# Optimization experiments

Hardware: AMD Instinct MI355X
Metric: run time of the kernel (lower is better)

## Reference

```python
import jax, jax.numpy as jnp
import numpy as np

N = 500_000
CHANNELS = 256
NUM_GRAPHS = 2048


def setup_inputs() -> dict:
    key = jax.random.key(0)
    k1, k2, k3 = jax.random.split(key, 3)
    features = jax.random.normal(k1, (N, CHANNELS), dtype=jnp.float32)
    batch = jnp.sort(jax.random.randint(k2, (N,), 0, NUM_GRAPHS, dtype=jnp.int64))
    batch = batch.at[-1].set(NUM_GRAPHS - 1)  # pin max so num_segments == NUM_GRAPHS
    W_att = jax.random.normal(k3, (CHANNELS, 1), dtype=jnp.float32) * (1.0 / np.sqrt(CHANNELS))
    b_att = jnp.zeros((1,), dtype=jnp.float32)
    return {"features": features, "batch": batch, "W_att": W_att, "b_att": b_att}


def reference(features, batch, W_att, b_att):
    # attention: Linear(channels, 1) -> Sigmoid, per node  [N, 1]
    weights = jax.nn.sigmoid(features @ W_att + b_att)
    # weighted per-graph sum: equivalent to the python loop over batch ids,
    # fused as a single segment reduction. num_segments = batch.max()+1 = NUM_GRAPHS.
    weighted = features * weights  # [N, C]
    out = jax.ops.segment_sum(weighted, batch, num_segments=NUM_GRAPHS)  # [B, C]
    return out
```

## Files before the change

kernel.cpp:

```cpp
#include <hip/hip_runtime.h>


constexpr int kChannels  = 256;
constexpr int kVecPerRow = kChannels / 4;

typedef float vfloat4 __attribute__((ext_vector_type(4)));

__device__ inline int lower_bound_i32(const int* __restrict__ b, int n, int v) {
    int lo = 0, hi = n;
    while (lo < hi) {
        int mid = (lo + hi) >> 1;
        if (b[mid] < v) lo = mid + 1; else hi = mid;
    }
    return lo;
}

__device__ inline float sigmoidf(float x) {
    return 1.0f / (1.0f + __expf(-x));
}

__global__ void hgp_seg_kernel(const float* __restrict__ features,
                               const int*   __restrict__ batch,
                               const float* __restrict__ W_att,
                               const float* __restrict__ b_att,
                               float*       __restrict__ out,
                               int n_nodes) {
    const int g    = blockIdx.x;
    const int wv   = threadIdx.x >> 6;
    const int lane = threadIdx.x & 63;

    const int seg_start = lower_bound_i32(batch, n_nodes, g);
    const int seg_end   = lower_bound_i32(batch, n_nodes, g + 1);
    const int seg_len   = seg_end - seg_start;

    const int q   = (seg_len + 3) >> 2;
    const int ws_ = seg_start + wv * q;
    const int we_ = min(ws_ + q, seg_end);

    const float4 w4  = reinterpret_cast<const float4*>(W_att)[lane];
    const float bias = b_att[0];
    const vfloat4* __restrict__ frow = reinterpret_cast<const vfloat4*>(features);

    float ax = 0.f, ay = 0.f, az = 0.f, aw = 0.f;

    int n = ws_;
    for (; n + 4 <= we_; n += 4) {
        const size_t base = (size_t)n * kVecPerRow + lane;
        vfloat4 r0 = __builtin_nontemporal_load(&frow[base]);
        vfloat4 r1 = __builtin_nontemporal_load(&frow[base + 1 * kVecPerRow]);
        vfloat4 r2 = __builtin_nontemporal_load(&frow[base + 2 * kVecPerRow]);
        vfloat4 r3 = __builtin_nontemporal_load(&frow[base + 3 * kVecPerRow]);

        float p0 = r0[0] * w4.x + r0[1] * w4.y + r0[2] * w4.z + r0[3] * w4.w;
        float p1 = r1[0] * w4.x + r1[1] * w4.y + r1[2] * w4.z + r1[3] * w4.w;
        float p2 = r2[0] * w4.x + r2[1] * w4.y + r2[2] * w4.z + r2[3] * w4.w;
        float p3 = r3[0] * w4.x + r3[1] * w4.y + r3[2] * w4.z + r3[3] * w4.w;

        #pragma unroll
        for (int off = 32; off > 0; off >>= 1) {
            p0 += __shfl_xor(p0, off, 64);
            p1 += __shfl_xor(p1, off, 64);
            p2 += __shfl_xor(p2, off, 64);
            p3 += __shfl_xor(p3, off, 64);
        }

        const float g0 = sigmoidf(p0 + bias);
        const float g1 = sigmoidf(p1 + bias);
        const float g2 = sigmoidf(p2 + bias);
        const float g3 = sigmoidf(p3 + bias);

        ax += r0[0] * g0 + r1[0] * g1 + r2[0] * g2 + r3[0] * g3;
        ay += r0[1] * g0 + r1[1] * g1 + r2[1] * g2 + r3[1] * g3;
        az += r0[2] * g0 + r1[2] * g1 + r2[2] * g2 + r3[2] * g3;
        aw += r0[3] * g0 + r1[3] * g1 + r2[3] * g2 + r3[3] * g3;
    }
    for (; n < we_; ++n) {
        vfloat4 r = __builtin_nontemporal_load(&frow[(size_t)n * kVecPerRow + lane]);
        float p = r[0] * w4.x + r[1] * w4.y + r[2] * w4.z + r[3] * w4.w;
        #pragma unroll
        for (int off = 32; off > 0; off >>= 1) p += __shfl_xor(p, off, 64);
        const float gg = sigmoidf(p + bias);
        ax += r[0] * gg; ay += r[1] * gg; az += r[2] * gg; aw += r[3] * gg;
    }

    __shared__ float lds[4][kChannels];
    lds[wv][lane * 4 + 0] = ax;
    lds[wv][lane * 4 + 1] = ay;
    lds[wv][lane * 4 + 2] = az;
    lds[wv][lane * 4 + 3] = aw;
    __syncthreads();

    const int t = threadIdx.x;
    const float s = lds[0][t] + lds[1][t] + lds[2][t] + lds[3][t];
    out[(size_t)g * kChannels + t] = s;
}

extern "C" void kernel_launch(void* const* d_in, const int* in_sizes, int n_in,
                              void* d_out, int out_size, void* d_ws, size_t ws_size,
                              hipStream_t stream) {
    const float* features = (const float*)d_in[0];
    const int*   batch    = (const int*)d_in[1];
    const float* W_att    = (const float*)d_in[2];
    const float* b_att    = (const float*)d_in[3];
    float*       out      = (float*)d_out;

    const int n_nodes    = in_sizes[1];
    const int num_graphs = out_size / kChannels;

    hgp_seg_kernel<<<num_graphs, 256, 0, stream>>>(features, batch, W_att, b_att,
                                                   out, n_nodes);
}
```

Before: 625.9 us.

## Split wave into 16-lane row groups with register double-buffered prefetch

Each wave now processes four rows at once, one per 16-lane group, with each lane holding four float4 chunks of its row. This cuts the dot-product reduction from six shuffle steps to four and computes one sigmoid per lane group. The next four rows are prefetched into registers while the current ones are processed, and partial sums are reduced across 16 LDS slots instead of 4. Launch bounds are added to limit register use. The cost is higher register pressure and a longer final LDS reduction.

```diff
diff --git a/kernel.cpp b/kernel.cpp
--- a/kernel.cpp
+++ b/kernel.cpp
@@ -15,19 +15,24 @@
     return lo;
 }
 
-__device__ inline float sigmoidf(float x) {
-    return 1.0f / (1.0f + __expf(-x));
+__device__ inline float sigmoidf(float x) { return 1.0f / (1.0f + __expf(-x)); }
+
+__device__ inline float dot4(vfloat4 a, vfloat4 b) {
+    return a[0] * b[0] + a[1] * b[1] + a[2] * b[2] + a[3] * b[3];
 }
 
-__global__ void hgp_seg_kernel(const float* __restrict__ features,
-                               const int*   __restrict__ batch,
-                               const float* __restrict__ W_att,
-                               const float* __restrict__ b_att,
-                               float*       __restrict__ out,
-                               int n_nodes) {
+__global__ __launch_bounds__(256, 2)
+void hgp_seg_kernel(const float* __restrict__ features,
+                    const int*   __restrict__ batch,
+                    const float* __restrict__ W_att,
+                    const float* __restrict__ b_att,
+                    float*       __restrict__ out,
+                    int n_nodes) {
     const int g    = blockIdx.x;
     const int wv   = threadIdx.x >> 6;
     const int lane = threadIdx.x & 63;
+    const int sub  = lane & 15;
+    const int grp  = lane >> 4;
 
     const int seg_start = lower_bound_i32(batch, n_nodes, g);
     const int seg_end   = lower_bound_i32(batch, n_nodes, g + 1);
@@ -37,61 +42,92 @@
     const int ws_ = seg_start + wv * q;
     const int we_ = min(ws_ + q, seg_end);
 
-    const float4 w4  = reinterpret_cast<const float4*>(W_att)[lane];
+    const vfloat4* __restrict__ frow = reinterpret_cast<const vfloat4*>(features);
+    const vfloat4* __restrict__ W4   = reinterpret_cast<const vfloat4*>(W_att);
+
+    const vfloat4 w0 = W4[sub];
+    const vfloat4 w1 = W4[sub + 16];
+    const vfloat4 w2 = W4[sub + 32];
+    const vfloat4 w3 = W4[sub + 48];
     const float bias = b_att[0];
-    const vfloat4* __restrict__ frow = reinterpret_cast<const vfloat4*>(features);
 
-    float ax = 0.f, ay = 0.f, az = 0.f, aw = 0.f;
+    vfloat4 a0 = 0.f, a1 = 0.f, a2 = 0.f, a3 = 0.f;
 
     int n = ws_;
-    for (; n + 4 <= we_; n += 4) {
-        const size_t base = (size_t)n * kVecPerRow + lane;
-        vfloat4 r0 = __builtin_nontemporal_load(&frow[base]);
-        vfloat4 r1 = __builtin_nontemporal_load(&frow[base + 1 * kVecPerRow]);
-        vfloat4 r2 = __builtin_nontemporal_load(&frow[base + 2 * kVecPerRow]);
-        vfloat4 r3 = __builtin_nontemporal_load(&frow[base + 3 * kVecPerRow]);
+    vfloat4 c0, c1, c2, c3;
 
-        float p0 = r0[0] * w4.x + r0[1] * w4.y + r0[2] * w4.z + r0[3] * w4.w;
-        float p1 = r1[0] * w4.x + r1[1] * w4.y + r1[2] * w4.z + r1[3] * w4.w;
-        float p2 = r2[0] * w4.x + r2[1] * w4.y + r2[2] * w4.z + r2[3] * w4.w;
-        float p3 = r3[0] * w4.x + r3[1] * w4.y + r3[2] * w4.z + r3[3] * w4.w;
-
-        #pragma unroll
-        for (int off = 32; off > 0; off >>= 1) {
-            p0 += __shfl_xor(p0, off, 64);
-            p1 += __shfl_xor(p1, off, 64);
-            p2 += __shfl_xor(p2, off, 64);
-            p3 += __shfl_xor(p3, off, 64);
-        }
-
-        const float g0 = sigmoidf(p0 + bias);
-        const float g1 = sigmoidf(p1 + bias);
-        const float g2 = sigmoidf(p2 + bias);
-        const float g3 = sigmoidf(p3 + bias);
-
-        ax += r0[0] * g0 + r1[0] * g1 + r2[0] * g2 + r3[0] * g3;
-        ay += r0[1] * g0 + r1[1] * g1 + r2[1] * g2 + r3[1] * g3;
-        az += r0[2] * g0 + r1[2] * g1 + r2[2] * g2 + r3[2] * g3;
-        aw += r0[3] * g0 + r1[3] * g1 + r2[3] * g2 + r3[3] * g3;
-    }
-    for (; n < we_; ++n) {
-        vfloat4 r = __builtin_nontemporal_load(&frow[(size_t)n * kVecPerRow + lane]);
-        float p = r[0] * w4.x + r[1] * w4.y + r[2] * w4.z + r[3] * w4.w;
-        #pragma unroll
-        for (int off = 32; off > 0; off >>= 1) p += __shfl_xor(p, off, 64);
-        const float gg = sigmoidf(p + bias);
-        ax += r[0] * gg; ay += r[1] * gg; az += r[2] * gg; aw += r[3] * gg;
+    if (n + 4 <= we_) {
+        const size_t rb = (size_t)(n + grp) * kVecPerRow + sub;
+        c0 = __builtin_nontemporal_load(&frow[rb]);
+        c1 = __builtin_nontemporal_load(&frow[rb + 16]);
+        c2 = __builtin_nontemporal_load(&frow[rb + 32]);
+        c3 = __builtin_nontemporal_load(&frow[rb + 48]);
     }
 
-    __shared__ float lds[4][kChannels];
-    lds[wv][lane * 4 + 0] = ax;
-    lds[wv][lane * 4 + 1] = ay;
-    lds[wv][lane * 4 + 2] = az;
-    lds[wv][lane * 4 + 3] = aw;
+    for (; n + 8 <= we_; n += 4) {
+        const size_t rb = (size_t)(n + 4 + grp) * kVecPerRow + sub;
+        vfloat4 x0 = __builtin_nontemporal_load(&frow[rb]);
+        vfloat4 x1 = __builtin_nontemporal_load(&frow[rb + 16]);
+        vfloat4 x2 = __builtin_nontemporal_load(&frow[rb + 32]);
+        vfloat4 x3 = __builtin_nontemporal_load(&frow[rb + 48]);
+
+        float p = dot4(c0, w0) + dot4(c1, w1) + dot4(c2, w2) + dot4(c3, w3);
+        p += __shfl_xor(p, 8, 64);
+        p += __shfl_xor(p, 4, 64);
+        p += __shfl_xor(p, 2, 64);
+        p += __shfl_xor(p, 1, 64);
+        const float gate = sigmoidf(p + bias);
+
+        a0 += c0 * gate; a1 += c1 * gate; a2 += c2 * gate; a3 += c3 * gate;
+
+        c0 = x0; c1 = x1; c2 = x2; c3 = x3;
+    }
+
+    if (n + 4 <= we_) {
+        float p = dot4(c0, w0) + dot4(c1, w1) + dot4(c2, w2) + dot4(c3, w3);
+        p += __shfl_xor(p, 8, 64);
+        p += __shfl_xor(p, 4, 64);
+        p += __shfl_xor(p, 2, 64);
+        p += __shfl_xor(p, 1, 64);
+        const float gate = sigmoidf(p + bias);
+        a0 += c0 * gate; a1 += c1 * gate; a2 += c2 * gate; a3 += c3 * gate;
+        n += 4;
+    }
+
+    if (n < we_) {
+        const int  row = n + grp;
+        const bool ok  = row < we_;
+        const size_t rb = (size_t)(ok ? row : we_ - 1) * kVecPerRow + sub;
+        vfloat4 t0 = __builtin_nontemporal_load(&frow[rb]);
+        vfloat4 t1 = __builtin_nontemporal_load(&frow[rb + 16]);
+        vfloat4 t2 = __builtin_nontemporal_load(&frow[rb + 32]);
+        vfloat4 t3 = __builtin_nontemporal_load(&frow[rb + 48]);
+        if (!ok) { t0 = 0.f; t1 = 0.f; t2 = 0.f; t3 = 0.f; }
+
+        float p = dot4(t0, w0) + dot4(t1, w1) + dot4(t2, w2) + dot4(t3, w3);
+        p += __shfl_xor(p, 8, 64);
+        p += __shfl_xor(p, 4, 64);
+        p += __shfl_xor(p, 2, 64);
+        p += __shfl_xor(p, 1, 64);
+        const float gate = sigmoidf(p + bias);
+        a0 += t0 * gate; a1 += t1 * gate; a2 += t2 * gate; a3 += t3 * gate;
+    }
+
+    __shared__ float lds[16][kChannels];
+    {
+        const int slot = wv * 4 + grp;
+        vfloat4* dst = reinterpret_cast<vfloat4*>(lds[slot]);
+        dst[sub]      = a0;
+        dst[sub + 16] = a1;
+        dst[sub + 32] = a2;
+        dst[sub + 48] = a3;
+    }
     __syncthreads();
 
     const int t = threadIdx.x;
-    const float s = lds[0][t] + lds[1][t] + lds[2][t] + lds[3][t];
+    float s = 0.f;
+    #pragma unroll
+    for (int k = 0; k < 16; ++k) s += lds[k][t];
     out[(size_t)g * kChannels + t] = s;
 }
 
```

Measured after the change: 626.6 us. Within noise of the previous version (+0.1%).
